# Performance work log

Measured on AMD Instinct MI355X. Metric: run time of the kernel, lower is better.

The kernel has to match this reference:

```python
import jax, jax.numpy as jnp
import numpy as np

B, S, D = 2, 2048, 1024
H, DK = 16, 64
DFF = 4096
WINDOW = 128
GLOBAL = 16
EPS = 1e-5


def _layer_norm(x, g, b):
    mu = jnp.mean(x, axis=-1, keepdims=True)
    var = jnp.var(x, axis=-1, keepdims=True)
    return (x - mu) * jax.lax.rsqrt(var + EPS) * g + b


def setup_inputs() -> dict:
    key = jax.random.key(0)
    ks = jax.random.split(key, 12)
    s = 0.02
    inp = {
        "x": jax.random.normal(ks[0], (B, S, D), dtype=jnp.float32),
        "Wq": jax.random.normal(ks[1], (D, D), jnp.float32) * s,
        "bq": jnp.zeros((D,), jnp.float32),
        "Wk": jax.random.normal(ks[2], (D, D), jnp.float32) * s,
        "bk": jnp.zeros((D,), jnp.float32),
        "Wv": jax.random.normal(ks[3], (D, D), jnp.float32) * s,
        "bv": jnp.zeros((D,), jnp.float32),
        "Wo": jax.random.normal(ks[4], (D, D), jnp.float32) * s,
        "bo": jnp.zeros((D,), jnp.float32),
        "ln1_g": jnp.ones((D,), jnp.float32),
        "ln1_b": jnp.zeros((D,), jnp.float32),
        "W1": jax.random.normal(ks[5], (D, DFF), jnp.float32) * s,
        "b1": jnp.zeros((DFF,), jnp.float32),
        "W2": jax.random.normal(ks[6], (DFF, D), jnp.float32) * s,
        "b2": jnp.zeros((D,), jnp.float32),
        "ln2_g": jnp.ones((D,), jnp.float32),
        "ln2_b": jnp.zeros((D,), jnp.float32),
    }
    return inp


def _local_global_mask(seq_len):
    # token i attends to j iff |i-j| <= WINDOW, or i < GLOBAL, or j < GLOBAL
    i = jnp.arange(seq_len)[:, None]
    j = jnp.arange(seq_len)[None, :]
    m = jnp.abs(i - j) <= WINDOW
    m = m | (i < GLOBAL) | (j < GLOBAL)
    return m  # [S, S] bool


def reference(x, Wq, bq, Wk, bk, Wv, bv, Wo, bo, ln1_g, ln1_b,
              W1, b1, W2, b2, ln2_g, ln2_b):
    # --- self-attention sublayer (pre-norm residual) ---
    xn = _layer_norm(x, ln1_g, ln1_b)
    q = (xn @ Wq + bq).reshape(B, S, H, DK).transpose(0, 2, 1, 3)  # [B,H,S,DK]
    k = (xn @ Wk + bk).reshape(B, S, H, DK).transpose(0, 2, 1, 3)
    v = (xn @ Wv + bv).reshape(B, S, H, DK).transpose(0, 2, 1, 3)

    scores = jnp.einsum('bhqd,bhkd->bhqk', q, k) / jnp.sqrt(jnp.float32(DK))
    mask = _local_global_mask(S)  # [S,S]
    scores = jnp.where(mask[None, None], scores, jnp.float32(-jnp.inf))
    attn = jax.nn.softmax(scores, axis=-1)
    out = jnp.einsum('bhqk,bhkd->bhqd', attn, v)
    out = out.transpose(0, 2, 1, 3).reshape(B, S, D)
    out = out @ Wo + bo
    x = x + out

    # --- feed-forward sublayer (pre-norm residual) ---
    xn2 = _layer_norm(x, ln2_g, ln2_b)
    h = jax.nn.gelu(xn2 @ W1 + b1, approximate=False)
    ff = h @ W2 + b2
    x = x + ff
    return x
```

## Files before the change

kernel.cpp:

```cpp
#include <hip/hip_runtime.h>
#include <stdint.h>


typedef unsigned short u16;
typedef unsigned int   u32;
typedef __attribute__((ext_vector_type(8))) short  short8;
typedef __attribute__((ext_vector_type(4))) float  f32x4;

#define S_LEN   2048
#define D_MODEL 1024
#define ROWS    4096

__device__ __forceinline__ float bf2f(u16 u) {
  union { u32 i; float f; } v; v.i = ((u32)u) << 16; return v.f;
}
__device__ __forceinline__ float bflo(u32 u) {
  union { u32 i; float f; } v; v.i = u << 16; return v.f;
}
__device__ __forceinline__ float bfhi(u32 u) {
  union { u32 i; float f; } v; v.i = u & 0xffff0000u; return v.f;
}
__device__ __forceinline__ u16 f2bf(float f) {
  union { float f; u32 i; } v; v.f = f;
  u32 r = v.i + 0x7fffu + ((v.i >> 16) & 1u);
  return (u16)(r >> 16);
}

__device__ __forceinline__ void gld_lds16(const u16* g, u16* l) {
  __attribute__((address_space(3))) u32* lp =
      reinterpret_cast<__attribute__((address_space(3))) u32*>(
          reinterpret_cast<uintptr_t>(l));
  const __attribute__((address_space(1))) u32* gp =
      reinterpret_cast<const __attribute__((address_space(1))) u32*>(
          reinterpret_cast<uintptr_t>(g));
  __builtin_amdgcn_global_load_lds(gp, lp, 16, 0, 0);
}


#define GBAR  asm volatile("s_barrier" ::: "memory")
#define LGKM(n) asm volatile("s_waitcnt lgkmcnt(" #n ")" ::: "memory")
#define VM(n)   asm volatile("s_waitcnt vmcnt(" #n ")" ::: "memory")
#define SB0   __builtin_amdgcn_sched_barrier(0)

#define STAGE_A(buf, t, hm) do {                                              \
    gld_lds16(pA##hm + (size_t)(t) * 64,      &Ald[buf][0][(hm)*4096 + ldst]);\
    gld_lds16(pA##hm + (size_t)(t) * 64 + 32, &Ald[buf][1][(hm)*4096 + ldst]);\
  } while (0)

#define STAGE_B(buf, t, hm) do {                                              \
    gld_lds16(pB##hm + (size_t)(t) * 64,      &Bld[buf][0][(hm)*4096 + ldst]);\
    gld_lds16(pB##hm + (size_t)(t) * 64 + 32, &Bld[buf][1][(hm)*4096 + ldst]);\
  } while (0)

#define READ_B(buf) do {                                                      \
    _Pragma("unroll") for (int nj = 0; nj < 4; ++nj) {                        \
      bfv[nj][0] = *(const short8*)&Bld[buf][0][brow + nj * 512];             \
      bfv[nj][1] = *(const short8*)&Bld[buf][1][brow + nj * 512]; }           \
  } while (0)

#define READ_A(buf, q) do {                                                   \
    af[(q)&1][0][0] = *(const short8*)&Ald[buf][0][arow + (2*(q)) * 512];     \
    af[(q)&1][0][1] = *(const short8*)&Ald[buf][1][arow + (2*(q)) * 512];     \
    af[(q)&1][1][0] = *(const short8*)&Ald[buf][0][arow + (2*(q)+1) * 512];   \
    af[(q)&1][1][1] = *(const short8*)&Ald[buf][1][arow + (2*(q)+1) * 512];   \
  } while (0)

#define MFMA_Q(q) do {                                                        \
    __builtin_amdgcn_s_setprio(1);                                            \
    _Pragma("unroll") for (int dm = 0; dm < 2; ++dm)                          \
    _Pragma("unroll") for (int kk = 0; kk < 2; ++kk)                          \
    _Pragma("unroll") for (int nj = 0; nj < 4; ++nj)                          \
      acc[2*(q)+dm][nj] = __builtin_amdgcn_mfma_f32_16x16x32_bf16(            \
          af[(q)&1][dm][kk], bfv[nj][kk], acc[2*(q)+dm][nj], 0, 0, 0);        \
    __builtin_amdgcn_s_setprio(0);                                            \
  } while (0)

template <int EPI, int KC, int LDK>
__global__ __launch_bounds__(512) void gemm256(
    const u16* __restrict__ A, const u16* __restrict__ Bt,
    const float* __restrict__ bias, u16* __restrict__ C0,
    u16* __restrict__ C1, int N)
{
  __shared__ __attribute__((aligned(16))) u16 Ald[2][2][256 * 32];
  __shared__ __attribute__((aligned(16))) u16 Bld[2][2][256 * 32];

  const int tid  = threadIdx.x;
  const int w    = tid >> 6;
  const int lane = tid & 63;
  const int wm   = w >> 2;
  const int wn   = w & 3;
  const int lm   = lane & 15;
  const int kq   = lane >> 4;
  const int bm   = blockIdx.y * 256;
  const int bn   = blockIdx.x * 256;
  const int kz   = blockIdx.z;

  const u16* Ak = A  + (size_t)kz * KC;
  const u16* Bk = Bt + (size_t)kz * KC;
  u16* C = kz ? C1 : C0;

  const int rslot = ((kq + (lm >> 1)) & 3) * 8;
  const int arow  = (wm * 128 + lm) * 32 + rslot;
  const int brow  = (wn * 64  + lm) * 32 + rslot;

  const int gcoff = (((lane & 3) - (lane >> 3)) & 3) * 8;
  const int srow  = w * 16 + (lane >> 2);
  const int ldst  = w * 512;

  const u16* pA0 = Ak + (size_t)(bm + srow) * LDK + gcoff;
  const u16* pA1 = pA0 + (size_t)128 * LDK;
  const u16* pB0 = Bk + (size_t)(bn + srow) * LDK + gcoff;
  const u16* pB1 = pB0 + (size_t)128 * LDK;

  f32x4 acc[8][4];
#pragma unroll
  for (int i = 0; i < 8; ++i)
#pragma unroll
    for (int j = 0; j < 4; ++j) acc[i][j] = (f32x4){0.f, 0.f, 0.f, 0.f};

  short8 af[2][2][2];
  short8 bfv[4][2];

  constexpr int P = KC >> 7;

  STAGE_B(0, 0, 0); STAGE_B(0, 0, 1);
  STAGE_A(0, 0, 0); STAGE_A(0, 0, 1);
  STAGE_B(1, 1, 0); STAGE_B(1, 1, 1);
  VM(4);
  GBAR;
  READ_A(0, 0);

  for (int i = 0; i < P - 1; ++i) {
    const int t1 = 2 * i + 1, t2 = 2 * i + 2, t3 = 2 * i + 3;
    GBAR; STAGE_A(1, t1, 0); READ_B(0); READ_A(0, 1); LGKM(4); SB0; MFMA_Q(0);
    GBAR; STAGE_A(1, t1, 1); READ_A(0, 2);            LGKM(4); SB0; MFMA_Q(1);
    GBAR; STAGE_B(0, t2, 0); READ_A(0, 3);            LGKM(4); SB0; MFMA_Q(2);
    VM(2);
    GBAR; STAGE_B(0, t2, 1); READ_A(1, 0);            LGKM(4); SB0; MFMA_Q(3);
    GBAR; STAGE_A(0, t2, 0); READ_B(1); READ_A(1, 1); LGKM(4); SB0; MFMA_Q(0);
    GBAR; STAGE_A(0, t2, 1); READ_A(1, 2);            LGKM(4); SB0; MFMA_Q(1);
    GBAR; STAGE_B(1, t3, 0); READ_A(1, 3);            LGKM(4); SB0; MFMA_Q(2);
    VM(2);
    GBAR; STAGE_B(1, t3, 1); READ_A(0, 0);            LGKM(4); SB0; MFMA_Q(3);
  }
  {
    const int t1 = 2 * P - 1;
    GBAR; STAGE_A(1, t1, 0); READ_B(0); READ_A(0, 1); LGKM(4); SB0; MFMA_Q(0);
    GBAR; STAGE_A(1, t1, 1); READ_A(0, 2);            LGKM(4); SB0; MFMA_Q(1);
    GBAR;                    READ_A(0, 3);            LGKM(4); SB0; MFMA_Q(2);
    VM(0);
    GBAR;                    READ_A(1, 0);            LGKM(4); SB0; MFMA_Q(3);
    GBAR;                    READ_B(1); READ_A(1, 1); LGKM(4); SB0; MFMA_Q(0);
    GBAR;                    READ_A(1, 2);            LGKM(4); SB0; MFMA_Q(1);
    GBAR;                    READ_A(1, 3);            LGKM(4); SB0; MFMA_Q(2);
    LGKM(0); SB0; MFMA_Q(3);
  }

  const int r0 = kq * 4;
#pragma unroll
  for (int mi = 0; mi < 8; ++mi) {
#pragma unroll
    for (int r = 0; r < 4; ++r) {
      const int grow = bm + wm * 128 + mi * 16 + r0 + r;
#pragma unroll
      for (int nj = 0; nj < 4; ++nj) {
        const int gcol = bn + wn * 64 + nj * 16 + lm;
        float v = acc[mi][nj][r];
        if (EPI < 2) v += bias[gcol];
        if (EPI == 1) v = 0.5f * v * (1.0f + erff(v * 0.70710678118654752f));
        C[(size_t)grow * N + gcol] = f2bf(v);
      }
    }
  }
}

__global__ __launch_bounds__(256) void reduce2(
    const u16* __restrict__ P0, const u16* __restrict__ P1,
    const float* __restrict__ bias, const float* res, float* out)
{
  const size_t base = ((size_t)blockIdx.x * 256 + threadIdx.x) * 8;
  const int col = (int)(base & 1023);
  uint4 p0 = *(const uint4*)(P0 + base);
  uint4 p1 = *(const uint4*)(P1 + base);
  float4 b0 = *(const float4*)(bias + col);
  float4 b1 = *(const float4*)(bias + col + 4);
  float4 r0 = *(const float4*)(res + base);
  float4 r1 = *(const float4*)(res + base + 4);
  float4 o0, o1;
  o0.x = bflo(p0.x) + bflo(p1.x) + b0.x + r0.x;
  o0.y = bfhi(p0.x) + bfhi(p1.x) + b0.y + r0.y;
  o0.z = bflo(p0.y) + bflo(p1.y) + b0.z + r0.z;
  o0.w = bfhi(p0.y) + bfhi(p1.y) + b0.w + r0.w;
  o1.x = bflo(p0.z) + bflo(p1.z) + b1.x + r1.x;
  o1.y = bfhi(p0.z) + bfhi(p1.z) + b1.y + r1.y;
  o1.z = bflo(p0.w) + bflo(p1.w) + b1.z + r1.z;
  o1.w = bfhi(p0.w) + bfhi(p1.w) + b1.w + r1.w;
  *(float4*)(out + base) = o0;
  *(float4*)(out + base + 4) = o1;
}

__global__ __launch_bounds__(256) void ln_kernel(
    const float* __restrict__ x, const float* __restrict__ g,
    const float* __restrict__ b, u16* __restrict__ o)
{
  const int row = blockIdx.x;
  const int t = threadIdx.x;
  float4 v = *(const float4*)(x + (size_t)row * D_MODEL + t * 4);
  float s  = v.x + v.y + v.z + v.w;
  float ss = v.x * v.x + v.y * v.y + v.z * v.z + v.w * v.w;
#pragma unroll
  for (int off = 32; off > 0; off >>= 1) {
    s  += __shfl_down(s, off);
    ss += __shfl_down(ss, off);
  }
  __shared__ float sm[4], ssm[4], stat[2];
  if ((t & 63) == 0) { sm[t >> 6] = s; ssm[t >> 6] = ss; }
  __syncthreads();
  if (t == 0) {
    float S = sm[0] + sm[1] + sm[2] + sm[3];
    float SS = ssm[0] + ssm[1] + ssm[2] + ssm[3];
    float mu = S * (1.0f / 1024.0f);
    float var = SS * (1.0f / 1024.0f) - mu * mu;
    stat[0] = mu;
    stat[1] = rsqrtf(fmaxf(var, 0.0f) + 1e-5f);
  }
  __syncthreads();
  const float mu = stat[0], rstd = stat[1];
  float4 gg = *(const float4*)(g + t * 4);
  float4 bb = *(const float4*)(b + t * 4);
  u16 o0 = f2bf((v.x - mu) * rstd * gg.x + bb.x);
  u16 o1 = f2bf((v.y - mu) * rstd * gg.y + bb.y);
  u16 o2 = f2bf((v.z - mu) * rstd * gg.z + bb.z);
  u16 o3 = f2bf((v.w - mu) * rstd * gg.w + bb.w);
  uint2 w;
  w.x = (u32)o0 | ((u32)o1 << 16);
  w.y = (u32)o2 | ((u32)o3 << 16);
  *(uint2*)(o + (size_t)row * D_MODEL + t * 4) = w;
}

__global__ __launch_bounds__(256) void attn_band(
    const u16* __restrict__ qkv, u16* __restrict__ out)
{
  const int t    = threadIdx.x;
  const int w    = t >> 6;
  const int lane = t & 63;
  const int m    = lane & 15;
  const int quad = lane >> 4;
  const int bh   = blockIdx.y;
  const int b    = bh >> 4, h = bh & 15;
  const int i0   = blockIdx.x * 64;
  const size_t bb = (size_t)b * S_LEN;

  __shared__ __attribute__((aligned(16))) u16 Ks[32 * 72];
  __shared__ __attribute__((aligned(16))) u16 Vt[64 * 40];
  __shared__ __attribute__((aligned(16))) u16 Ps[4][16 * 40];

  const u16* qrow = qkv + (bb + i0 + 16 * w + m) * 3072 + h * 64;
  const short8 aq0 = *(const short8*)(qrow + quad * 8);
  const short8 aq1 = *(const short8*)(qrow + 32 + quad * 8);

  f32x4 Ov[4];
#pragma unroll
  for (int td = 0; td < 4; ++td) Ov[td] = (f32x4){0.f, 0.f, 0.f, 0.f};
  float mP[4] = {-1e30f, -1e30f, -1e30f, -1e30f};
  float lS[4] = {0.f, 0.f, 0.f, 0.f};

  const int iB = i0 + 16 * w + quad * 4;

  const int lo = max(32, i0 - 128);
  const int hi = min(S_LEN, i0 + 192);
  const int nChunks = 1 + (hi - lo) / 32;

  const int skr = t >> 3;
  const int skc = (t & 7) * 8;

  for (int c = 0; c < nChunks; ++c) {
    const int j0 = (c == 0) ? 0 : lo + (c - 1) * 32;
    __syncthreads();
    {
      const u16* src = qkv + (bb + j0 + skr) * 3072 + 1024 + h * 64 + skc;
      uint4 kk = *(const uint4*)src;
      uint4 vv = *(const uint4*)(src + 1024);
      *(uint4*)&Ks[skr * 72 + skc] = kk;
      const u16 vs[8] = {
        (u16)(vv.x & 0xffffu), (u16)(vv.x >> 16),
        (u16)(vv.y & 0xffffu), (u16)(vv.y >> 16),
        (u16)(vv.z & 0xffffu), (u16)(vv.z >> 16),
        (u16)(vv.w & 0xffffu), (u16)(vv.w >> 16)};
#pragma unroll
      for (int i = 0; i < 8; ++i) Vt[(skc + i) * 40 + skr] = vs[i];
    }
    __syncthreads();

    const short8 b00 = *(const short8*)&Ks[m * 72 + quad * 8];
    const short8 b01 = *(const short8*)&Ks[m * 72 + 32 + quad * 8];
    const short8 b10 = *(const short8*)&Ks[(16 + m) * 72 + quad * 8];
    const short8 b11 = *(const short8*)&Ks[(16 + m) * 72 + 32 + quad * 8];
    f32x4 s0 = (f32x4){0.f, 0.f, 0.f, 0.f};
    f32x4 s1 = (f32x4){0.f, 0.f, 0.f, 0.f};
    s0 = __builtin_amdgcn_mfma_f32_16x16x32_bf16(aq0, b00, s0, 0, 0, 0);
    s0 = __builtin_amdgcn_mfma_f32_16x16x32_bf16(aq1, b01, s0, 0, 0, 0);
    s1 = __builtin_amdgcn_mfma_f32_16x16x32_bf16(aq0, b10, s1, 0, 0, 0);
    s1 = __builtin_amdgcn_mfma_f32_16x16x32_bf16(aq1, b11, s1, 0, 0, 0);

    const int jA = j0 + m, jB = j0 + 16 + m;
#pragma unroll
    for (int r = 0; r < 4; ++r) {
      const int iG = iB + r;
      const int da = iG - jA, db = iG - jB;
      s0[r] = ((jA < 16) || (da >= -128 && da <= 128)) ? s0[r] * 0.125f : -1e30f;
      s1[r] = ((jB < 16) || (db >= -128 && db <= 128)) ? s1[r] * 0.125f : -1e30f;
    }

    float al[4];
#pragma unroll
    for (int r = 0; r < 4; ++r) {
      float mx = fmaxf(s0[r], s1[r]);
      mx = fmaxf(mx, __shfl_xor(mx, 1, 16));
      mx = fmaxf(mx, __shfl_xor(mx, 2, 16));
      mx = fmaxf(mx, __shfl_xor(mx, 4, 16));
      mx = fmaxf(mx, __shfl_xor(mx, 8, 16));
      const float mn = fmaxf(mP[r], mx);
      al[r] = __expf(mP[r] - mn);
      mP[r] = mn;
      const float p0 = __expf(s0[r] - mn);
      const float p1 = __expf(s1[r] - mn);
      float ps = p0 + p1;
      ps += __shfl_xor(ps, 1, 16);
      ps += __shfl_xor(ps, 2, 16);
      ps += __shfl_xor(ps, 4, 16);
      ps += __shfl_xor(ps, 8, 16);
      lS[r] = lS[r] * al[r] + ps;
      Ps[w][(quad * 4 + r) * 40 + m]      = f2bf(p0);
      Ps[w][(quad * 4 + r) * 40 + 16 + m] = f2bf(p1);
    }
#pragma unroll
    for (int td = 0; td < 4; ++td)
#pragma unroll
      for (int r = 0; r < 4; ++r) Ov[td][r] *= al[r];

    const short8 pa = *(const short8*)&Ps[w][m * 40 + quad * 8];
#pragma unroll
    for (int td = 0; td < 4; ++td) {
      const short8 bv = *(const short8*)&Vt[(td * 16 + m) * 40 + quad * 8];
      Ov[td] = __builtin_amdgcn_mfma_f32_16x16x32_bf16(pa, bv, Ov[td], 0, 0, 0);
    }
  }

  if (i0 + 16 * w >= 16) {
    float inv[4];
#pragma unroll
    for (int r = 0; r < 4; ++r) inv[r] = 1.0f / lS[r];
#pragma unroll
    for (int td = 0; td < 4; ++td)
#pragma unroll
      for (int r = 0; r < 4; ++r)
        out[(bb + iB + r) * 1024 + h * 64 + td * 16 + m] =
            f2bf(Ov[td][r] * inv[r]);
  }
}

__global__ __launch_bounds__(256) void attn_gpart(
    const u16* __restrict__ qkv, float* __restrict__ Obuf,
    float* __restrict__ mbuf, float* __restrict__ lbuf)
{
  const int t    = threadIdx.x;
  const int w    = t >> 6;
  const int lane = t & 63;
  const int m    = lane & 15;
  const int quad = lane >> 4;
  const int kb   = blockIdx.x;
  const int bh   = blockIdx.y;
  const int b    = bh >> 4, h = bh & 15;
  const size_t bb = (size_t)b * S_LEN;

  __shared__ __attribute__((aligned(16))) u16 Ks[4][32 * 72];
  __shared__ __attribute__((aligned(16))) u16 Vt[4][64 * 40];
  __shared__ __attribute__((aligned(16))) u16 Ps[4][16 * 40];

  const u16* qrow = qkv + (bb + m) * 3072 + h * 64;
  const short8 aq0 = *(const short8*)(qrow + quad * 8);
  const short8 aq1 = *(const short8*)(qrow + 32 + quad * 8);

  f32x4 Ov[4];
#pragma unroll
  for (int td = 0; td < 4; ++td) Ov[td] = (f32x4){0.f, 0.f, 0.f, 0.f};
  float mP[4] = {-1e30f, -1e30f, -1e30f, -1e30f};
  float lS[4] = {0.f, 0.f, 0.f, 0.f};

  const int srow = lane >> 1;
  const int sd   = (lane & 1) * 32;

  for (int c = 0; c < 2; ++c) {
    const int j0 = kb * 256 + w * 64 + c * 32;
    {
      const u16* src = qkv + (bb + j0 + srow) * 3072 + 1024 + h * 64 + sd;
      uint4 k0 = *(const uint4*)(src);
      uint4 k1 = *(const uint4*)(src + 8);
      uint4 k2 = *(const uint4*)(src + 16);
      uint4 k3 = *(const uint4*)(src + 24);
      *(uint4*)&Ks[w][srow * 72 + sd]      = k0;
      *(uint4*)&Ks[w][srow * 72 + sd + 8]  = k1;
      *(uint4*)&Ks[w][srow * 72 + sd + 16] = k2;
      *(uint4*)&Ks[w][srow * 72 + sd + 24] = k3;
#pragma unroll
      for (int q4 = 0; q4 < 4; ++q4) {
        uint4 vv = *(const uint4*)(src + 1024 + q4 * 8);
        const u16 vs[8] = {
          (u16)(vv.x & 0xffffu), (u16)(vv.x >> 16),
          (u16)(vv.y & 0xffffu), (u16)(vv.y >> 16),
          (u16)(vv.z & 0xffffu), (u16)(vv.z >> 16),
          (u16)(vv.w & 0xffffu), (u16)(vv.w >> 16)};
#pragma unroll
        for (int i = 0; i < 8; ++i)
          Vt[w][(sd + q4 * 8 + i) * 40 + srow] = vs[i];
      }
    }

    const short8 b00 = *(const short8*)&Ks[w][m * 72 + quad * 8];
    const short8 b01 = *(const short8*)&Ks[w][m * 72 + 32 + quad * 8];
    const short8 b10 = *(const short8*)&Ks[w][(16 + m) * 72 + quad * 8];
    const short8 b11 = *(const short8*)&Ks[w][(16 + m) * 72 + 32 + quad * 8];
    f32x4 s0 = (f32x4){0.f, 0.f, 0.f, 0.f};
    f32x4 s1 = (f32x4){0.f, 0.f, 0.f, 0.f};
    s0 = __builtin_amdgcn_mfma_f32_16x16x32_bf16(aq0, b00, s0, 0, 0, 0);
    s0 = __builtin_amdgcn_mfma_f32_16x16x32_bf16(aq1, b01, s0, 0, 0, 0);
    s1 = __builtin_amdgcn_mfma_f32_16x16x32_bf16(aq0, b10, s1, 0, 0, 0);
    s1 = __builtin_amdgcn_mfma_f32_16x16x32_bf16(aq1, b11, s1, 0, 0, 0);

    float al[4];
#pragma unroll
    for (int r = 0; r < 4; ++r) {
      const float v0 = s0[r] * 0.125f, v1 = s1[r] * 0.125f;
      float mx = fmaxf(v0, v1);
      mx = fmaxf(mx, __shfl_xor(mx, 1, 16));
      mx = fmaxf(mx, __shfl_xor(mx, 2, 16));
      mx = fmaxf(mx, __shfl_xor(mx, 4, 16));
      mx = fmaxf(mx, __shfl_xor(mx, 8, 16));
      const float mn = fmaxf(mP[r], mx);
      al[r] = __expf(mP[r] - mn);
      mP[r] = mn;
      const float p0 = __expf(v0 - mn);
      const float p1 = __expf(v1 - mn);
      float ps = p0 + p1;
      ps += __shfl_xor(ps, 1, 16);
      ps += __shfl_xor(ps, 2, 16);
      ps += __shfl_xor(ps, 4, 16);
      ps += __shfl_xor(ps, 8, 16);
      lS[r] = lS[r] * al[r] + ps;
      Ps[w][(quad * 4 + r) * 40 + m]      = f2bf(p0);
      Ps[w][(quad * 4 + r) * 40 + 16 + m] = f2bf(p1);
    }
#pragma unroll
    for (int td = 0; td < 4; ++td)
#pragma unroll
      for (int r = 0; r < 4; ++r) Ov[td][r] *= al[r];

    const short8 pa = *(const short8*)&Ps[w][m * 40 + quad * 8];
#pragma unroll
    for (int td = 0; td < 4; ++td) {
      const short8 bv = *(const short8*)&Vt[w][(td * 16 + m) * 40 + quad * 8];
      Ov[td] = __builtin_amdgcn_mfma_f32_16x16x32_bf16(pa, bv, Ov[td], 0, 0, 0);
    }
  }

  const int p = kb * 4 + w;
  const size_t ob = ((size_t)(bh * 32 + p)) * 16 * 64;
#pragma unroll
  for (int td = 0; td < 4; ++td)
#pragma unroll
    for (int r = 0; r < 4; ++r)
      Obuf[ob + (size_t)(quad * 4 + r) * 64 + td * 16 + m] = Ov[td][r];
  if (m == 0) {
    const int mb = (bh * 32 + p) * 16;
#pragma unroll
    for (int r = 0; r < 4; ++r) {
      mbuf[mb + quad * 4 + r] = mP[r];
      lbuf[mb + quad * 4 + r] = lS[r];
    }
  }
}

__global__ __launch_bounds__(256) void attn_gcombine(
    const float* __restrict__ Obuf, const float* __restrict__ mbuf,
    const float* __restrict__ lbuf, u16* __restrict__ out)
{
  const int bh = blockIdx.x;
  const int b  = bh >> 4, h = bh & 15;
  const int t  = threadIdx.x;
  const int q  = t >> 4;
  const int d0 = (t & 15) * 4;
  const int mb = bh * 32 * 16;

  float mv[32];
  float M = -1e30f;
#pragma unroll
  for (int p = 0; p < 32; ++p) {
    mv[p] = mbuf[mb + p * 16 + q];
    M = fmaxf(M, mv[p]);
  }
  float L = 0.f;
  float4 acc = {0.f, 0.f, 0.f, 0.f};
#pragma unroll
  for (int p = 0; p < 32; ++p) {
    const float wp = __expf(mv[p] - M);
    L += lbuf[mb + p * 16 + q] * wp;
    float4 o = *(const float4*)&Obuf[(((size_t)(bh * 32 + p)) * 16 + q) * 64 + d0];
    acc.x += wp * o.x; acc.y += wp * o.y;
    acc.z += wp * o.z; acc.w += wp * o.w;
  }
  const float inv = 1.0f / L;
  uint2 wv;
  wv.x = (u32)f2bf(acc.x * inv) | ((u32)f2bf(acc.y * inv) << 16);
  wv.y = (u32)f2bf(acc.z * inv) | ((u32)f2bf(acc.w * inv) << 16);
  *(uint2*)(out + ((size_t)b * S_LEN + q) * 1024 + h * 64 + d0) = wv;
}

__global__ __launch_bounds__(256) void prep_all(
    const float* __restrict__ Wq, const float* __restrict__ Wk,
    const float* __restrict__ Wv, const float* __restrict__ Wo,
    const float* __restrict__ W1, const float* __restrict__ W2,
    const float* __restrict__ bq, const float* __restrict__ bk,
    const float* __restrict__ bv,
    u16* __restrict__ WQKVT, u16* __restrict__ WOT,
    u16* __restrict__ W1T, u16* __restrict__ W2T,
    float* __restrict__ BQKV)
{
  const int gb = blockIdx.x;
  const int t = threadIdx.x;
  if (gb >= 3072) {
    const int i = (gb - 3072) * 256 + t;
    if (i < 1024) BQKV[i] = bq[i];
    else if (i < 2048) BQKV[i] = bk[i - 1024];
    else BQKV[i] = bv[i - 2048];
    return;
  }
  const float* in; u16* outp; int R, Cc, bx, by;
  if (gb < 1024) {
    const int seg = gb >> 8, local = gb & 255;
    bx = local & 15; by = local >> 4; R = 1024; Cc = 1024;
    in   = (seg == 0) ? Wq : (seg == 1) ? Wk : (seg == 2) ? Wv : Wo;
    outp = (seg < 3) ? WQKVT + (size_t)seg * 1024 * 1024 : WOT;
  } else if (gb < 2048) {
    const int local = gb - 1024;
    bx = local & 63; by = local >> 6; R = 1024; Cc = 4096;
    in = W1; outp = W1T;
  } else {
    const int local = gb - 2048;
    bx = local & 15; by = local >> 4; R = 4096; Cc = 1024;
    in = W2; outp = W2T;
  }

  __shared__ u16 tile[64][65];
  const int tr = by * 64, tc = bx * 64;
  const int lr = t >> 2, lc0 = (t & 3) * 16;
  const float* src = in + (size_t)(tr + lr) * Cc + tc + lc0;
  float4 a0 = *(const float4*)(src);
  float4 a1 = *(const float4*)(src + 4);
  float4 a2 = *(const float4*)(src + 8);
  float4 a3 = *(const float4*)(src + 12);
  const float vals[16] = {a0.x, a0.y, a0.z, a0.w, a1.x, a1.y, a1.z, a1.w,
                          a2.x, a2.y, a2.z, a2.w, a3.x, a3.y, a3.z, a3.w};
#pragma unroll
  for (int q = 0; q < 16; ++q) tile[lr][lc0 + q] = f2bf(vals[q]);
  __syncthreads();
  u16* dst = outp + (size_t)(tc + lr) * R + tr + lc0;
  u32 w[8];
#pragma unroll
  for (int q = 0; q < 8; ++q)
    w[q] = (u32)tile[lc0 + 2 * q][lr] | ((u32)tile[lc0 + 2 * q + 1][lr] << 16);
  uint4 s0; s0.x = w[0]; s0.y = w[1]; s0.z = w[2]; s0.w = w[3];
  uint4 s1; s1.x = w[4]; s1.y = w[5]; s1.z = w[6]; s1.w = w[7];
  *(uint4*)dst = s0;
  *(uint4*)(dst + 8) = s1;
}

static const size_t OFF_WQKVT = 0;
static const size_t OFF_WOT   = OFF_WQKVT + (size_t)3072 * 1024 * 2;
static const size_t OFF_W1T   = OFF_WOT   + (size_t)1024 * 1024 * 2;
static const size_t OFF_W2T   = OFF_W1T   + (size_t)4096 * 1024 * 2;
static const size_t OFF_BQKV  = OFF_W2T   + (size_t)1024 * 4096 * 2;
static const size_t OFF_XN    = OFF_BQKV  + 16384;
static const size_t OFF_QKV   = OFF_XN    + (size_t)4096 * 1024 * 2;
static const size_t OFF_AO    = OFF_QKV   + (size_t)4096 * 3072 * 2;
static const size_t OFF_H     = OFF_QKV;

extern "C" void kernel_launch(void* const* d_in, const int* in_sizes, int n_in,
                              void* d_out, int out_size, void* d_ws, size_t ws_size,
                              hipStream_t stream)
{
  const float* x   = (const float*)d_in[0];
  const float* Wq  = (const float*)d_in[1];
  const float* bq  = (const float*)d_in[2];
  const float* Wk  = (const float*)d_in[3];
  const float* bk  = (const float*)d_in[4];
  const float* Wv  = (const float*)d_in[5];
  const float* bv  = (const float*)d_in[6];
  const float* Wo  = (const float*)d_in[7];
  const float* bo  = (const float*)d_in[8];
  const float* g1  = (const float*)d_in[9];
  const float* be1 = (const float*)d_in[10];
  const float* W1  = (const float*)d_in[11];
  const float* b1  = (const float*)d_in[12];
  const float* W2  = (const float*)d_in[13];
  const float* b2  = (const float*)d_in[14];
  const float* g2  = (const float*)d_in[15];
  const float* be2 = (const float*)d_in[16];
  float* outf = (float*)d_out;
  char* ws = (char*)d_ws;

  u16*   WQKVT = (u16*)(ws + OFF_WQKVT);
  u16*   WOT   = (u16*)(ws + OFF_WOT);
  u16*   W1T   = (u16*)(ws + OFF_W1T);
  u16*   W2T   = (u16*)(ws + OFF_W2T);
  float* BQKV  = (float*)(ws + OFF_BQKV);
  u16*   XN    = (u16*)(ws + OFF_XN);
  u16*   QKV   = (u16*)(ws + OFF_QKV);
  u16*   AO    = (u16*)(ws + OFF_AO);
  u16*   Hbuf  = (u16*)(ws + OFF_H);
  float* X1    = outf;
  u16* PWo0 = (u16*)(ws + OFF_QKV);
  u16* PWo1 = PWo0 + (size_t)4096 * 1024;
  u16* PW20 = (u16*)(ws + OFF_W1T);
  u16* PW21 = (u16*)(ws + OFF_XN);
  float* GO = (float*)(ws + OFF_XN);
  float* GM = GO + (size_t)32 * 32 * 16 * 64;
  float* GL = GM + 32 * 32 * 16;

  const dim3 blk(256);
  const dim3 blk512(512);
  prep_all<<<dim3(3084), blk, 0, stream>>>(Wq, Wk, Wv, Wo, W1, W2, bq, bk, bv,
                                           WQKVT, WOT, W1T, W2T, BQKV);

  ln_kernel<<<dim3(ROWS), blk, 0, stream>>>(x, g1, be1, XN);
  gemm256<0, 1024, 1024><<<dim3(12, 16, 1), blk512, 0, stream>>>(
      XN, WQKVT, BQKV, QKV, QKV, 3072);
  attn_band<<<dim3(32, 32), blk, 0, stream>>>(QKV, AO);
  attn_gpart<<<dim3(8, 32), blk, 0, stream>>>(QKV, GO, GM, GL);
  attn_gcombine<<<dim3(32), blk, 0, stream>>>(GO, GM, GL, AO);
  gemm256<2, 512, 1024><<<dim3(4, 16, 2), blk512, 0, stream>>>(
      AO, WOT, nullptr, PWo0, PWo1, 1024);
  reduce2<<<dim3(2048), blk, 0, stream>>>(PWo0, PWo1, bo, x, X1);

  ln_kernel<<<dim3(ROWS), blk, 0, stream>>>(X1, g2, be2, XN);
  gemm256<1, 1024, 1024><<<dim3(16, 16, 1), blk512, 0, stream>>>(
      XN, W1T, b1, Hbuf, Hbuf, 4096);
  gemm256<2, 2048, 4096><<<dim3(4, 16, 2), blk512, 0, stream>>>(
      Hbuf, W2T, nullptr, PW20, PW21, 1024);
  reduce2<<<dim3(2048), blk, 0, stream>>>(PW20, PW21, b2, X1, outf);
}
```

Measured before the change: 346.6 us.

## Split Wo GEMM four ways along K and fuse reduction with second LayerNorm

```diff
diff --git a/kernel.cpp b/kernel.cpp
--- a/kernel.cpp
+++ b/kernel.cpp
@@ -79,7 +79,8 @@
 __global__ __launch_bounds__(512) void gemm256(
     const u16* __restrict__ A, const u16* __restrict__ Bt,
     const float* __restrict__ bias, u16* __restrict__ C0,
-    u16* __restrict__ C1, int N)
+    u16* __restrict__ C1, u16* __restrict__ C2, u16* __restrict__ C3,
+    int N)
 {
   __shared__ __attribute__((aligned(16))) u16 Ald[2][2][256 * 32];
   __shared__ __attribute__((aligned(16))) u16 Bld[2][2][256 * 32];
@@ -97,7 +98,7 @@
 
   const u16* Ak = A  + (size_t)kz * KC;
   const u16* Bk = Bt + (size_t)kz * KC;
-  u16* C = kz ? C1 : C0;
+  u16* C = (kz == 0) ? C0 : (kz == 1) ? C1 : (kz == 2) ? C2 : C3;
 
   const int rslot = ((kq + (lm >> 1)) & 3) * 8;
   const int arow  = (wm * 128 + lm) * 32 + rslot;
@@ -197,6 +198,62 @@
   o1.w = bfhi(p0.w) + bfhi(p1.w) + b1.w + r1.w;
   *(float4*)(out + base) = o0;
   *(float4*)(out + base + 4) = o1;
+}
+
+__global__ __launch_bounds__(256) void reduce4_ln(
+    const u16* __restrict__ P0, const u16* __restrict__ P1,
+    const u16* __restrict__ P2, const u16* __restrict__ P3,
+    const float* __restrict__ bias, const float* __restrict__ res,
+    const float* __restrict__ g, const float* __restrict__ bp,
+    float* __restrict__ X1, u16* __restrict__ XN)
+{
+  const int row = blockIdx.x;
+  const int t = threadIdx.x;
+  const size_t base = (size_t)row * D_MODEL + t * 4;
+  const int col = t * 4;
+  uint2 a0 = *(const uint2*)(P0 + base);
+  uint2 a1 = *(const uint2*)(P1 + base);
+  uint2 a2 = *(const uint2*)(P2 + base);
+  uint2 a3 = *(const uint2*)(P3 + base);
+  float4 bb = *(const float4*)(bias + col);
+  float4 rr = *(const float4*)(res + base);
+  float4 y;
+  y.x = bflo(a0.x) + bflo(a1.x) + bflo(a2.x) + bflo(a3.x) + bb.x + rr.x;
+  y.y = bfhi(a0.x) + bfhi(a1.x) + bfhi(a2.x) + bfhi(a3.x) + bb.y + rr.y;
+  y.z = bflo(a0.y) + bflo(a1.y) + bflo(a2.y) + bflo(a3.y) + bb.z + rr.z;
+  y.w = bfhi(a0.y) + bfhi(a1.y) + bfhi(a2.y) + bfhi(a3.y) + bb.w + rr.w;
+  *(float4*)(X1 + base) = y;
+
+  float s  = y.x + y.y + y.z + y.w;
+  float ss = y.x * y.x + y.y * y.y + y.z * y.z + y.w * y.w;
+#pragma unroll
+  for (int off = 32; off > 0; off >>= 1) {
+    s  += __shfl_down(s, off);
+    ss += __shfl_down(ss, off);
+  }
+  __shared__ float sm[4], ssm[4], stat[2];
+  if ((t & 63) == 0) { sm[t >> 6] = s; ssm[t >> 6] = ss; }
+  __syncthreads();
+  if (t == 0) {
+    float S = sm[0] + sm[1] + sm[2] + sm[3];
+    float SS = ssm[0] + ssm[1] + ssm[2] + ssm[3];
+    float mu = S * (1.0f / 1024.0f);
+    float var = SS * (1.0f / 1024.0f) - mu * mu;
+    stat[0] = mu;
+    stat[1] = rsqrtf(fmaxf(var, 0.0f) + 1e-5f);
+  }
+  __syncthreads();
+  const float mu = stat[0], rstd = stat[1];
+  float4 gg = *(const float4*)(g + col);
+  float4 be = *(const float4*)(bp + col);
+  u16 o0 = f2bf((y.x - mu) * rstd * gg.x + be.x);
+  u16 o1 = f2bf((y.y - mu) * rstd * gg.y + be.y);
+  u16 o2 = f2bf((y.z - mu) * rstd * gg.z + be.z);
+  u16 o3 = f2bf((y.w - mu) * rstd * gg.w + be.w);
+  uint2 wv;
+  wv.x = (u32)o0 | ((u32)o1 << 16);
+  wv.y = (u32)o2 | ((u32)o3 << 16);
+  *(uint2*)(XN + base) = wv;
 }
 
 __global__ __launch_bounds__(256) void ln_kernel(
@@ -621,6 +678,8 @@
   float* X1    = outf;
   u16* PWo0 = (u16*)(ws + OFF_QKV);
   u16* PWo1 = PWo0 + (size_t)4096 * 1024;
+  u16* PWo2 = PWo1 + (size_t)4096 * 1024;
+  u16* PWo3 = (u16*)(ws + OFF_XN);
   u16* PW20 = (u16*)(ws + OFF_W1T);
   u16* PW21 = (u16*)(ws + OFF_XN);
   float* GO = (float*)(ws + OFF_XN);
@@ -634,18 +693,18 @@
 
   ln_kernel<<<dim3(ROWS), blk, 0, stream>>>(x, g1, be1, XN);
   gemm256<0, 1024, 1024><<<dim3(12, 16, 1), blk512, 0, stream>>>(
-      XN, WQKVT, BQKV, QKV, QKV, 3072);
+      XN, WQKVT, BQKV, QKV, QKV, QKV, QKV, 3072);
   attn_band<<<dim3(32, 32), blk, 0, stream>>>(QKV, AO);
   attn_gpart<<<dim3(8, 32), blk, 0, stream>>>(QKV, GO, GM, GL);
   attn_gcombine<<<dim3(32), blk, 0, stream>>>(GO, GM, GL, AO);
-  gemm256<2, 512, 1024><<<dim3(4, 16, 2), blk512, 0, stream>>>(
-      AO, WOT, nullptr, PWo0, PWo1, 1024);
-  reduce2<<<dim3(2048), blk, 0, stream>>>(PWo0, PWo1, bo, x, X1);
-
-  ln_kernel<<<dim3(ROWS), blk, 0, stream>>>(X1, g2, be2, XN);
+  gemm256<2, 256, 1024><<<dim3(4, 16, 4), blk512, 0, stream>>>(
+      AO, WOT, nullptr, PWo0, PWo1, PWo2, PWo3, 1024);
+  reduce4_ln<<<dim3(ROWS), blk, 0, stream>>>(PWo0, PWo1, PWo2, PWo3,
+                                             bo, x, g2, be2, X1, XN);
+
   gemm256<1, 1024, 1024><<<dim3(16, 16, 1), blk512, 0, stream>>>(
-      XN, W1T, b1, Hbuf, Hbuf, 4096);
+      XN, W1T, b1, Hbuf, Hbuf, Hbuf, Hbuf, 4096);
   gemm256<2, 2048, 4096><<<dim3(4, 16, 2), blk512, 0, stream>>>(
-      Hbuf, W2T, nullptr, PW20, PW21, 1024);
+      Hbuf, W2T, nullptr, PW20, PW21, PW21, PW21, 1024);
   reduce2<<<dim3(2048), blk, 0, stream>>>(PW20, PW21, b2, X1, outf);
 }
```

After: 348.2 us. Within noise of the previous version (+0.5%).
